# Optimization experiments

Hardware: AMD Instinct MI355X
Metric: run time of the kernel (lower is better)

## Reference

```python
import jax, jax.numpy as jnp
import numpy as np

B, S, D, U = 64, 2048, 512, 512

def setup_inputs() -> dict:
    key = jax.random.key(0)
    ks = jax.random.split(key, 8)
    query = jax.random.normal(ks[0], (B, D), dtype=jnp.float32)
    values = jax.random.normal(ks[1], (B, S, D), dtype=jnp.float32)
    # Keras Dense params (glorot-like scale), with biases (Dense default use_bias=True)
    W1 = jax.random.normal(ks[2], (D, U), dtype=jnp.float32) / np.sqrt(D)
    b1 = jnp.zeros((U,), dtype=jnp.float32)
    W2 = jax.random.normal(ks[3], (D, U), dtype=jnp.float32) / np.sqrt(D)
    b2 = jnp.zeros((U,), dtype=jnp.float32)
    V = jax.random.normal(ks[4], (U, 1), dtype=jnp.float32) / np.sqrt(U)
    bv = jnp.zeros((1,), dtype=jnp.float32)
    return {"query": query, "values": values, "W1": W1, "b1": b1,
            "W2": W2, "b2": b2, "V": V, "bv": bv}

def reference(query, values, W1, b1, W2, b2, V, bv) -> jnp.ndarray:
    # query: [B, D], values: [B, S, D]
    q_proj = query @ W1 + b1                      # [B, U]
    v_proj = jnp.einsum('bsd,du->bsu', values, W2) + b2  # [B, S, U]
    h = jnp.tanh(q_proj[:, None, :] + v_proj)     # [B, S, U]
    scores = jnp.einsum('bsu,uo->bso', h, V) + bv # [B, S, 1]
    attn = jax.nn.softmax(scores, axis=1)         # softmax over sequence axis
    context = jnp.sum(attn * values, axis=1)      # [B, D]
    return context
```

## Files before the change

### kernel.cpp

```cpp
#include <hip/hip_runtime.h>
#include <hip/hip_bf16.h>

#define BB 64
#define SS 2048
#define DD 512
#define UU 512
#define BS (BB*SS)

typedef __attribute__((ext_vector_type(8))) short bf16x8;
typedef __attribute__((ext_vector_type(16))) float f32x16;

static __device__ __forceinline__ unsigned short f2bf(float x) {
    union { float f; unsigned int u; } v; v.f = x;
    unsigned int r = v.u + 0x7FFFu + ((v.u >> 16) & 1u);
    return (unsigned short)(r >> 16);
}

__global__ void k_prep(const float* __restrict__ W2, unsigned short* __restrict__ W2F,
                       const float* __restrict__ query, const float* __restrict__ W1,
                       const float* __restrict__ b1, const float* __restrict__ b2,
                       float* __restrict__ qpb) {
    __shared__ float tile[64][65];
    const int t = threadIdx.x;
    if (blockIdx.x < 64) {
        const int ti = blockIdx.x >> 3;
        const int tj = blockIdx.x & 7;
        #pragma unroll
        for (int i = 0; i < 16; ++i) {
            int e = i*256 + t;
            int dr = e >> 6, uc = e & 63;
            tile[dr][uc] = W2[(size_t)(ti*64+dr)*UU + tj*64+uc];
        }
        __syncthreads();
        const int ksl = t >> 6, ln = t & 63;
        const int lh = ln >> 5, l31 = ln & 31;
        #pragma unroll
        for (int ntl = 0; ntl < 2; ++ntl) {
            const int ks = ti*4 + ksl;
            const int ntile = tj*2 + ntl;
            bf16x8 g;
            #pragma unroll
            for (int j = 0; j < 8; ++j)
                g[j] = (short)f2bf(tile[ksl*16 + lh*8 + j][ntl*32 + l31]);
            *(bf16x8*)&W2F[(size_t)(((ks*16 + ntile)*64 + ln) * 8)] = g;
        }
    } else {
        const int b = blockIdx.x - 64;
        float a0 = 0.f, a1 = 0.f;
        for (int d = 0; d < DD; ++d) {
            float q = query[b*DD + d];
            a0 += q * W1[(size_t)d*UU + t];
            a1 += q * W1[(size_t)d*UU + t + 256];
        }
        qpb[b*UU + t]       = a0 + b1[t]     + b2[t];
        qpb[b*UU + t + 256] = a1 + b1[t+256] + b2[t+256];
    }
}

__launch_bounds__(256, 2)
__global__ void k_scores(const float* __restrict__ values,
                         const unsigned short* __restrict__ W2F,
                         const float* __restrict__ qpb,
                         const float* __restrict__ Vw,
                         float* __restrict__ pm, float* __restrict__ pl,
                         float* __restrict__ pv) {
    __shared__ unsigned short Albuf[64*512];
    const int t   = threadIdx.x;
    const int blk = blockIdx.x;
    const int m0  = blk * 64;
    const int b   = blk >> 5;
    const int wave = t >> 6, lane = t & 63;
    const int ln31 = lane & 31, half = lane >> 5;

    const bf16x8* Bp = (const bf16x8*)W2F;
    bf16x8 bfr[2][4];
    #pragma unroll
    for (int nt = 0; nt < 4; ++nt)
        bfr[0][nt] = Bp[(0*16 + wave*4 + nt)*64 + lane];
    #pragma unroll
    for (int nt = 0; nt < 4; ++nt)
        bfr[1][nt] = Bp[(1*16 + wave*4 + nt)*64 + lane];

    float qv[4], vw[4];
    #pragma unroll
    for (int nt = 0; nt < 4; ++nt) {
        int n = wave*128 + nt*32 + ln31;
        qv[nt] = qpb[b*UU + n];
        vw[nt] = Vw[n];
    }

    const float* src = values + (size_t)m0 * DD;
    #pragma unroll
    for (int i = 0; i < 16; ++i) {
        int gf  = i*256 + t;
        int row = gf >> 6;
        int g   = gf & 63;
        const float4 f0 = *(const float4*)(src + (size_t)row*DD + g*8);
        const float4 f1 = *(const float4*)(src + (size_t)row*DD + g*8 + 4);
        bf16x8 pk;
        pk[0] = (short)f2bf(f0.x); pk[1] = (short)f2bf(f0.y);
        pk[2] = (short)f2bf(f0.z); pk[3] = (short)f2bf(f0.w);
        pk[4] = (short)f2bf(f1.x); pk[5] = (short)f2bf(f1.y);
        pk[6] = (short)f2bf(f1.z); pk[7] = (short)f2bf(f1.w);
        *(bf16x8*)&Albuf[row*512 + ((g ^ (row & 7)) << 3)] = pk;
    }
    __syncthreads();

    f32x16 acc[2][4];
    #pragma unroll
    for (int mt = 0; mt < 2; ++mt)
        #pragma unroll
        for (int nt = 0; nt < 4; ++nt)
            #pragma unroll
            for (int r = 0; r < 16; ++r)
                acc[mt][nt][r] = 0.f;

    const int xm = ln31 & 7;
    #pragma unroll 4
    for (int ks = 0; ks < 32; ++ks) {
        const int cur = ks & 1;
        const int g8 = (((ks*2 + half) ^ xm) << 3);
        bf16x8 a0 = *(const bf16x8*)&Albuf[ln31*512 + g8];
        bf16x8 a1 = *(const bf16x8*)&Albuf[16384 + ln31*512 + g8];
        #pragma unroll
        for (int nt = 0; nt < 4; ++nt) {
            acc[0][nt] = __builtin_amdgcn_mfma_f32_32x32x16_bf16(a0, bfr[cur][nt], acc[0][nt], 0, 0, 0);
            acc[1][nt] = __builtin_amdgcn_mfma_f32_32x32x16_bf16(a1, bfr[cur][nt], acc[1][nt], 0, 0, 0);
        }
        #pragma unroll
        for (int nt = 0; nt < 4; ++nt)
            bfr[cur][nt] = Bp[((ks+2)*16 + wave*4 + nt)*64 + lane];
    }

    float sacc[2][16];
    #pragma unroll
    for (int mt = 0; mt < 2; ++mt)
        #pragma unroll
        for (int r = 0; r < 16; ++r)
            sacc[mt][r] = 0.f;
    #pragma unroll
    for (int nt = 0; nt < 4; ++nt) {
        const float q = qv[nt], w = vw[nt];
        #pragma unroll
        for (int mt = 0; mt < 2; ++mt)
            #pragma unroll
            for (int r = 0; r < 16; ++r) {
                float x = q + acc[mt][nt][r];
                float e = __expf(x + x);
                float rc = __builtin_amdgcn_rcpf(e + 1.f);
                sacc[mt][r] = fmaf(fmaf(-2.f, rc, 1.f), w, sacc[mt][r]);
            }
    }

    __syncthreads();
    float* sred = (float*)Albuf;
    #pragma unroll
    for (int mt = 0; mt < 2; ++mt)
        #pragma unroll
        for (int r = 0; r < 16; ++r) {
            float v = sacc[mt][r];
            v += __shfl_xor(v, 1);
            v += __shfl_xor(v, 2);
            v += __shfl_xor(v, 4);
            v += __shfl_xor(v, 8);
            v += __shfl_xor(v, 16);
            if (ln31 == 0)
                sred[wave*64 + mt*32 + (r & 3) + 8*(r >> 2) + 4*half] = v;
        }
    __syncthreads();

    if (t < 64) {
        float s = sred[t] + sred[64 + t] + sred[128 + t] + sred[192 + t];
        float m = s;
        #pragma unroll
        for (int off = 32; off; off >>= 1) m = fmaxf(m, __shfl_xor(m, off));
        float p = __expf(s - m);
        float l = p;
        #pragma unroll
        for (int off = 32; off; off >>= 1) l += __shfl_xor(l, off);
        sred[256 + t] = p;
        if (t == 0) { pm[blk] = m; pl[blk] = l; }
    }
    __syncthreads();

    float2 cacc = make_float2(0.f, 0.f);
    const float* vrow = values + (size_t)m0*DD + t*2;
    #pragma unroll 8
    for (int i = 0; i < 64; ++i) {
        float p = sred[256 + i];
        float2 v = *(const float2*)(vrow + (size_t)i*DD);
        cacc.x = fmaf(p, v.x, cacc.x);
        cacc.y = fmaf(p, v.y, cacc.y);
    }
    *(float2*)&pv[(size_t)blk*DD + t*2] = cacc;
}

__global__ void k_finish(const float* __restrict__ pv, const float* __restrict__ pm,
                         const float* __restrict__ pl, float* __restrict__ out) {
    __shared__ float sm_[32], sl_[32], sw[32];
    const int b = blockIdx.x, t = threadIdx.x;
    if (t < 32) { sm_[t] = pm[b*32 + t]; sl_[t] = pl[b*32 + t]; }
    __syncthreads();
    float M = -1e30f;
    #pragma unroll
    for (int c = 0; c < 32; ++c) M = fmaxf(M, sm_[c]);
    float L = 0.f;
    #pragma unroll
    for (int c = 0; c < 32; ++c) L += sl_[c] * __expf(sm_[c] - M);
    if (t < 32) sw[t] = __expf(sm_[t] - M) / L;
    __syncthreads();
    float2 a = make_float2(0.f, 0.f);
    #pragma unroll 4
    for (int c = 0; c < 32; ++c) {
        float w = sw[c];
        float2 v = *(const float2*)&pv[(size_t)(b*32 + c)*DD + t*2];
        a.x = fmaf(w, v.x, a.x);
        a.y = fmaf(w, v.y, a.y);
    }
    *(float2*)&out[(size_t)b*DD + t*2] = a;
}

extern "C" void kernel_launch(void* const* d_in, const int* in_sizes, int n_in,
                              void* d_out, int out_size, void* d_ws, size_t ws_size,
                              hipStream_t stream) {
    const float* query  = (const float*)d_in[0];
    const float* values = (const float*)d_in[1];
    const float* W1     = (const float*)d_in[2];
    const float* b1     = (const float*)d_in[3];
    const float* W2     = (const float*)d_in[4];
    const float* b2     = (const float*)d_in[5];
    const float* Vw     = (const float*)d_in[6];

    char* ws = (char*)d_ws;
    unsigned short* W2F = (unsigned short*)ws;
    float* qpb = (float*)(ws + 557056);
    float* pm  = (float*)(ws + 557056 + 131072);
    float* pl  = (float*)(ws + 557056 + 131072 + 8192);
    float* pv  = (float*)(ws + 557056 + 131072 + 16384);

    k_prep<<<128, 256, 0, stream>>>(W2, W2F, query, W1, b1, b2, qpb);
    k_scores<<<BS/64, 256, 0, stream>>>(values, W2F, qpb, Vw, pm, pl, pv);
    k_finish<<<BB, 256, 0, stream>>>(pv, pm, pl, (float*)d_out);
}
```

Baseline: 507.9 us.

## Split score GEMM across eight waves and parallelize the query projection

```diff
diff --git a/kernel.cpp b/kernel.cpp
--- a/kernel.cpp
+++ b/kernel.cpp
@@ -21,6 +21,7 @@
                        const float* __restrict__ b1, const float* __restrict__ b2,
                        float* __restrict__ qpb) {
     __shared__ float tile[64][65];
+    __shared__ float qs[512];
     const int t = threadIdx.x;
     if (blockIdx.x < 64) {
         const int ti = blockIdx.x >> 3;
@@ -45,19 +46,25 @@
             *(bf16x8*)&W2F[(size_t)(((ks*16 + ntile)*64 + ln) * 8)] = g;
         }
     } else {
-        const int b = blockIdx.x - 64;
-        float a0 = 0.f, a1 = 0.f;
-        for (int d = 0; d < DD; ++d) {
-            float q = query[b*DD + d];
-            a0 += q * W1[(size_t)d*UU + t];
-            a1 += q * W1[(size_t)d*UU + t + 256];
-        }
-        qpb[b*UU + t]       = a0 + b1[t]     + b2[t];
-        qpb[b*UU + t + 256] = a1 + b1[t+256] + b2[t+256];
-    }
-}
-
-__launch_bounds__(256, 2)
+        const int idx = blockIdx.x - 64;
+        const int b  = idx >> 1;
+        const int uh = idx & 1;
+        const int u  = uh*256 + t;
+        if (t < 256) { qs[t] = query[b*DD + t]; qs[t+256] = query[b*DD + t + 256]; }
+        __syncthreads();
+        float p0 = 0.f, p1 = 0.f, p2 = 0.f, p3 = 0.f;
+        #pragma unroll 2
+        for (int d = 0; d < DD; d += 4) {
+            p0 = fmaf(qs[d+0], W1[(size_t)(d+0)*UU + u], p0);
+            p1 = fmaf(qs[d+1], W1[(size_t)(d+1)*UU + u], p1);
+            p2 = fmaf(qs[d+2], W1[(size_t)(d+2)*UU + u], p2);
+            p3 = fmaf(qs[d+3], W1[(size_t)(d+3)*UU + u], p3);
+        }
+        qpb[b*UU + u] = (p0 + p1) + (p2 + p3) + b1[u] + b2[u];
+    }
+}
+
+__launch_bounds__(512, 4)
 __global__ void k_scores(const float* __restrict__ values,
                          const unsigned short* __restrict__ W2F,
                          const float* __restrict__ qpb,
@@ -73,26 +80,26 @@
     const int ln31 = lane & 31, half = lane >> 5;
 
     const bf16x8* Bp = (const bf16x8*)W2F;
-    bf16x8 bfr[2][4];
-    #pragma unroll
-    for (int nt = 0; nt < 4; ++nt)
-        bfr[0][nt] = Bp[(0*16 + wave*4 + nt)*64 + lane];
-    #pragma unroll
-    for (int nt = 0; nt < 4; ++nt)
-        bfr[1][nt] = Bp[(1*16 + wave*4 + nt)*64 + lane];
-
-    float qv[4], vw[4];
-    #pragma unroll
-    for (int nt = 0; nt < 4; ++nt) {
-        int n = wave*128 + nt*32 + ln31;
+    bf16x8 bfr[2][2];
+    #pragma unroll
+    for (int nt = 0; nt < 2; ++nt)
+        bfr[0][nt] = Bp[(0*16 + wave*2 + nt)*64 + lane];
+    #pragma unroll
+    for (int nt = 0; nt < 2; ++nt)
+        bfr[1][nt] = Bp[(1*16 + wave*2 + nt)*64 + lane];
+
+    float qv[2], vw[2];
+    #pragma unroll
+    for (int nt = 0; nt < 2; ++nt) {
+        int n = wave*64 + nt*32 + ln31;
         qv[nt] = qpb[b*UU + n];
         vw[nt] = Vw[n];
     }
 
     const float* src = values + (size_t)m0 * DD;
     #pragma unroll
-    for (int i = 0; i < 16; ++i) {
-        int gf  = i*256 + t;
+    for (int i = 0; i < 8; ++i) {
+        int gf  = i*512 + t;
         int row = gf >> 6;
         int g   = gf & 63;
         const float4 f0 = *(const float4*)(src + (size_t)row*DD + g*8);
@@ -106,11 +113,11 @@
     }
     __syncthreads();
 
-    f32x16 acc[2][4];
+    f32x16 acc[2][2];
     #pragma unroll
     for (int mt = 0; mt < 2; ++mt)
         #pragma unroll
-        for (int nt = 0; nt < 4; ++nt)
+        for (int nt = 0; nt < 2; ++nt)
             #pragma unroll
             for (int r = 0; r < 16; ++r)
                 acc[mt][nt][r] = 0.f;
@@ -123,42 +130,37 @@
         bf16x8 a0 = *(const bf16x8*)&Albuf[ln31*512 + g8];
         bf16x8 a1 = *(const bf16x8*)&Albuf[16384 + ln31*512 + g8];
         #pragma unroll
-        for (int nt = 0; nt < 4; ++nt) {
+        for (int nt = 0; nt < 2; ++nt) {
             acc[0][nt] = __builtin_amdgcn_mfma_f32_32x32x16_bf16(a0, bfr[cur][nt], acc[0][nt], 0, 0, 0);
             acc[1][nt] = __builtin_amdgcn_mfma_f32_32x32x16_bf16(a1, bfr[cur][nt], acc[1][nt], 0, 0, 0);
         }
         #pragma unroll
-        for (int nt = 0; nt < 4; ++nt)
-            bfr[cur][nt] = Bp[((ks+2)*16 + wave*4 + nt)*64 + lane];
-    }
-
-    float sacc[2][16];
-    #pragma unroll
-    for (int mt = 0; mt < 2; ++mt)
-        #pragma unroll
-        for (int r = 0; r < 16; ++r)
-            sacc[mt][r] = 0.f;
-    #pragma unroll
-    for (int nt = 0; nt < 4; ++nt) {
-        const float q = qv[nt], w = vw[nt];
-        #pragma unroll
-        for (int mt = 0; mt < 2; ++mt)
+        for (int nt = 0; nt < 2; ++nt)
+            bfr[cur][nt] = Bp[((ks+2)*16 + wave*2 + nt)*64 + lane];
+    }
+
+    __syncthreads();
+    float* sred = (float*)Albuf;
+
+    #pragma unroll
+    for (int mt = 0; mt < 2; ++mt) {
+        float s[16];
+        #pragma unroll
+        for (int r = 0; r < 16; ++r) s[r] = 0.f;
+        #pragma unroll
+        for (int nt = 0; nt < 2; ++nt) {
+            const float q = qv[nt], w = vw[nt];
             #pragma unroll
             for (int r = 0; r < 16; ++r) {
                 float x = q + acc[mt][nt][r];
                 float e = __expf(x + x);
                 float rc = __builtin_amdgcn_rcpf(e + 1.f);
-                sacc[mt][r] = fmaf(fmaf(-2.f, rc, 1.f), w, sacc[mt][r]);
+                s[r] = fmaf(fmaf(-2.f, rc, 1.f), w, s[r]);
             }
-    }
-
-    __syncthreads();
-    float* sred = (float*)Albuf;
-    #pragma unroll
-    for (int mt = 0; mt < 2; ++mt)
+        }
         #pragma unroll
         for (int r = 0; r < 16; ++r) {
-            float v = sacc[mt][r];
+            float v = s[r];
             v += __shfl_xor(v, 1);
             v += __shfl_xor(v, 2);
             v += __shfl_xor(v, 4);
@@ -167,10 +169,13 @@
             if (ln31 == 0)
                 sred[wave*64 + mt*32 + (r & 3) + 8*(r >> 2) + 4*half] = v;
         }
+    }
     __syncthreads();
 
     if (t < 64) {
-        float s = sred[t] + sred[64 + t] + sred[128 + t] + sred[192 + t];
+        float s = 0.f;
+        #pragma unroll
+        for (int w = 0; w < 8; ++w) s += sred[w*64 + t];
         float m = s;
         #pragma unroll
         for (int off = 32; off; off >>= 1) m = fmaxf(m, __shfl_xor(m, off));
@@ -178,21 +183,31 @@
         float l = p;
         #pragma unroll
         for (int off = 32; off; off >>= 1) l += __shfl_xor(l, off);
-        sred[256 + t] = p;
+        sred[512 + t] = p;
         if (t == 0) { pm[blk] = m; pl[blk] = l; }
     }
     __syncthreads();
 
+    const int tt = t & 255, th = t >> 8;
+    const float* sp = sred + 512;
     float2 cacc = make_float2(0.f, 0.f);
-    const float* vrow = values + (size_t)m0*DD + t*2;
+    const float* vrow = values + (size_t)m0*DD + tt*2;
     #pragma unroll 8
-    for (int i = 0; i < 64; ++i) {
-        float p = sred[256 + i];
-        float2 v = *(const float2*)(vrow + (size_t)i*DD);
+    for (int i = 0; i < 32; ++i) {
+        const int rowi = th*32 + i;
+        float p = sp[rowi];
+        float2 v = *(const float2*)(vrow + (size_t)rowi*DD);
         cacc.x = fmaf(p, v.x, cacc.x);
         cacc.y = fmaf(p, v.y, cacc.y);
     }
-    *(float2*)&pv[(size_t)blk*DD + t*2] = cacc;
+    float2* cred = (float2*)(sred + 576);
+    if (th == 1) cred[tt] = cacc;
+    __syncthreads();
+    if (th == 0) {
+        float2 o = cred[tt];
+        cacc.x += o.x; cacc.y += o.y;
+        *(float2*)&pv[(size_t)blk*DD + tt*2] = cacc;
+    }
 }
 
 __global__ void k_finish(const float* __restrict__ pv, const float* __restrict__ pm,
@@ -238,7 +253,7 @@
     float* pl  = (float*)(ws + 557056 + 131072 + 8192);
     float* pv  = (float*)(ws + 557056 + 131072 + 16384);
 
-    k_prep<<<128, 256, 0, stream>>>(W2, W2F, query, W1, b1, b2, qpb);
-    k_scores<<<BS/64, 256, 0, stream>>>(values, W2F, qpb, Vw, pm, pl, pv);
+    k_prep<<<192, 256, 0, stream>>>(W2, W2F, query, W1, b1, b2, qpb);
+    k_scores<<<BS/64, 512, 0, stream>>>(values, W2F, qpb, Vw, pm, pl, pv);
     k_finish<<<BB, 256, 0, stream>>>(pv, pm, pl, (float*)d_out);
 }
```

Measured after the change: 499.5 us. No clear change (-1.6%).
